# Optimization experiments

Hardware: AMD Instinct MI355X
Metric: run time of the kernel (lower is better)

The kernel has to match this reference:

```python
import jax, jax.numpy as jnp
import numpy as np

N_HEADS = 8
MAX_PARTS = 8
TOKENS_PER_PART = 64
NUM_BLOCKS = 6
D_MODEL = 256
LN_EPS = 1e-5


def layernorm(x, w, b):
    mu = jnp.mean(x, axis=-1, keepdims=True)
    var = jnp.var(x, axis=-1, keepdims=True)
    return (x - mu) * jax.lax.rsqrt(var + LN_EPS) * w + b


def mha(q, k, v, in_w, in_b, out_w, out_b):
    # torch nn.MultiheadAttention: packed in_proj [3D, D], out_proj [D, D]
    D = q.shape[-1]
    dh = D // N_HEADS
    wq, wk, wv = in_w[:D], in_w[D:2 * D], in_w[2 * D:]
    bq, bk, bv = in_b[:D], in_b[D:2 * D], in_b[2 * D:]
    qp = q @ wq.T + bq  # [B, Sq, D]
    kp = k @ wk.T + bk
    vp = v @ wv.T + bv
    B, Sq, _ = qp.shape
    Sk = kp.shape[1]
    qh = qp.reshape(B, Sq, N_HEADS, dh).transpose(0, 2, 1, 3)
    kh = kp.reshape(B, Sk, N_HEADS, dh).transpose(0, 2, 1, 3)
    vh = vp.reshape(B, Sk, N_HEADS, dh).transpose(0, 2, 1, 3)
    scores = jnp.einsum('bhqd,bhkd->bhqk', qh, kh) / jnp.sqrt(jnp.asarray(dh, qp.dtype))
    attn = jax.nn.softmax(scores, axis=-1)
    out = jnp.einsum('bhqk,bhkd->bhqd', attn, vh)
    out = out.transpose(0, 2, 1, 3).reshape(B, Sq, D)
    return out @ out_w.T + out_b


def setup_inputs() -> dict:
    key = jax.random.key(0)
    ks = jax.random.split(key, 16)
    s = 0.02
    return {
        'feat': jax.random.normal(ks[0], (64, 49, 512), jnp.float32),
        'img_proj_w': jax.random.normal(ks[1], (256, 512), jnp.float32) * s,
        'img_proj_b': jnp.zeros((256,), jnp.float32),
        'init_part_tokens': jax.random.normal(ks[2], (512, 256), jnp.float32),
        'part_id_emb': jax.random.normal(ks[3], (8, 256), jnp.float32),
        'local_in_w': jax.random.normal(ks[4], (768, 256), jnp.float32) * s,
        'local_in_b': jnp.zeros((768,), jnp.float32),
        'local_out_w': jax.random.normal(ks[5], (256, 256), jnp.float32) * s,
        'local_out_b': jnp.zeros((256,), jnp.float32),
        'cross_in_w': jax.random.normal(ks[6], (768, 256), jnp.float32) * s,
        'cross_in_b': jnp.zeros((768,), jnp.float32),
        'cross_out_w': jax.random.normal(ks[7], (256, 256), jnp.float32) * s,
        'cross_out_b': jnp.zeros((256,), jnp.float32),
        'norm1_w': jnp.ones((6, 256), jnp.float32),
        'norm1_b': jnp.zeros((6, 256), jnp.float32),
        'norm2_w': jnp.ones((6, 256), jnp.float32),
        'norm2_b': jnp.zeros((6, 256), jnp.float32),
        'coord_w': jax.random.normal(ks[8], (3, 256), jnp.float32) * s,
        'coord_b': jnp.zeros((3,), jnp.float32),
    }


def reference(feat, img_proj_w, img_proj_b, init_part_tokens, part_id_emb,
              local_in_w, local_in_b, local_out_w, local_out_b,
              cross_in_w, cross_in_b, cross_out_w, cross_out_b,
              norm1_w, norm1_b, norm2_w, norm2_b, coord_w, coord_b):
    B = feat.shape[0]
    P, T, D = MAX_PARTS, TOKENS_PER_PART, D_MODEL
    img_tokens = feat @ img_proj_w.T + img_proj_b  # [B, 49, D]
    # broadcast part-id embedding over tokens_per_part
    pid = jnp.repeat(part_id_emb, T, axis=0)  # [P*T, D]
    st = jnp.broadcast_to(init_part_tokens + pid, (B, P * T, D))
    for i in range(NUM_BLOCKS):
        # block-diagonal local attention: fold parts into batch dim
        parts = st.reshape(B * P, T, D)
        local = mha(parts, parts, parts, local_in_w, local_in_b, local_out_w, local_out_b)
        local = local.reshape(B, P * T, D)
        st = layernorm(st + local, norm1_w[i], norm1_b[i])
        cross = mha(st, img_tokens, img_tokens, cross_in_w, cross_in_b, cross_out_w, cross_out_b)
        st = layernorm(st + cross, norm2_w[i], norm2_b[i])
    coords = st @ coord_w.T + coord_b
    return coords.reshape(B, P, T, 3)
```

## Files before the change

kernel.cpp:

```cpp
#include <hip/hip_runtime.h>
#include <hip/hip_bf16.h>


#define B_     64
#define P_     8
#define T_     64
#define S_     512
#define D_     256
#define H_     8
#define DH_    32
#define NIMG_  49
#define M_ST   32768
#define M_IMG  3136
#define OSTR   264

#define AS1 __attribute__((address_space(1)))
#define AS3 __attribute__((address_space(3)))

typedef short bf16x8 __attribute__((ext_vector_type(8)));
typedef float f32x4  __attribute__((ext_vector_type(4)));

__device__ inline uint f2b_pk(float x, float y) {
    uint bx = __float_as_uint(x), by = __float_as_uint(y);
    bx = (bx + 0x7FFFu + ((bx >> 16) & 1u)) >> 16;
    by = (by + 0x7FFFu + ((by >> 16) & 1u)) >> 16;
    return bx | (by << 16);
}
__device__ inline ushort f2b(float x) {
    uint b = __float_as_uint(x);
    return (ushort)((b + 0x7FFFu + ((b >> 16) & 1u)) >> 16);
}
__device__ inline float b2f(ushort u) {
    return __uint_as_float(((uint)u) << 16);
}

__global__ __launch_bounds__(256) void cvt_bf16x4(
    const float4* __restrict__ in, uint2* __restrict__ out, int n4)
{
    int i = blockIdx.x * 256 + threadIdx.x;
    if (i < n4) {
        float4 v = in[i];
        out[i] = make_uint2(f2b_pk(v.x, v.y), f2b_pk(v.z, v.w));
    }
}

__global__ __launch_bounds__(256) void gemm_bf16(
    const ushort* __restrict__ A,
    const ushort* __restrict__ W,
    const float*  __restrict__ bias,
    ushort*       __restrict__ C,
    int M, int N, int K)
{
    __shared__ ushort smem[128 * 128];
    ushort* Asm = smem;
    ushort* Bsm = smem + 4096;

    const int tid  = threadIdx.x;
    const int lane = tid & 63;
    const int wave = tid >> 6;
    const int wr = wave >> 1, wc = wave & 1;
    const int row0 = blockIdx.x * 128, col0 = blockIdx.y * 128;

    f32x4 acc[4][4] = {};

    const int skc = (tid & 3) * 8;
    const int sr0 = tid >> 2;
    const int fr  = lane & 15;
    const int g   = lane >> 4;

    for (int k0 = 0; k0 < K; k0 += 32) {
        #pragma unroll
        for (int i = 0; i < 2; ++i) {
            const int r = sr0 + i * 64;
            const int e = (tid + i * 256) * 8;
            int ra = row0 + r; if (ra >= M) ra = M - 1;
            __builtin_amdgcn_global_load_lds(
                (const AS1 void*)(A + (size_t)ra * K + k0 + skc),
                (AS3 void*)&Asm[e], 16, 0, 0);
            __builtin_amdgcn_global_load_lds(
                (const AS1 void*)(W + (size_t)(col0 + r) * K + k0 + skc),
                (AS3 void*)&Bsm[e], 16, 0, 0);
        }
        __syncthreads();

        bf16x8 af[4], bf[4];
        #pragma unroll
        for (int i = 0; i < 4; ++i)
            af[i] = *reinterpret_cast<const bf16x8*>(&Asm[(wr * 64 + i * 16 + fr) * 32 + g * 8]);
        #pragma unroll
        for (int j = 0; j < 4; ++j)
            bf[j] = *reinterpret_cast<const bf16x8*>(&Bsm[(wc * 64 + j * 16 + fr) * 32 + g * 8]);
        #pragma unroll
        for (int i = 0; i < 4; ++i)
            #pragma unroll
            for (int j = 0; j < 4; ++j)
                acc[i][j] = __builtin_amdgcn_mfma_f32_16x16x32_bf16(
                    af[i], bf[j], acc[i][j], 0, 0, 0);
        __syncthreads();
    }

    float bn[4];
    #pragma unroll
    for (int j = 0; j < 4; ++j) bn[j] = bias[col0 + wc * 64 + j * 16 + fr];

    #pragma unroll
    for (int i = 0; i < 4; ++i)
        #pragma unroll
        for (int j = 0; j < 4; ++j)
            #pragma unroll
            for (int r = 0; r < 4; ++r)
                smem[(wr * 64 + i * 16 + g * 4 + r) * 128 + wc * 64 + j * 16 + fr] =
                    f2b(acc[i][j][r] + bn[j]);
    __syncthreads();

    #pragma unroll
    for (int it = 0; it < 8; ++it) {
        const int elem = (it * 256 + tid) * 8;
        const int lrow = elem >> 7, lcol = elem & 127;
        const int m = row0 + lrow;
        if (m < M)
            *reinterpret_cast<uint4*>(&C[(size_t)m * N + col0 + lcol]) =
                *reinterpret_cast<const uint4*>(&smem[elem]);
    }
}

__global__ __launch_bounds__(512, 4) void gemm_bf16_big(
    const ushort* __restrict__ A,
    const ushort* __restrict__ W,
    const float*  __restrict__ bias,
    ushort*       __restrict__ C,
    int N, int K)
{
    __shared__ ushort smem[16384];
    ushort* Asm = smem;
    ushort* Bsm = smem + 8192;

    const int tid  = threadIdx.x;
    const int lane = tid & 63;
    const int wave = tid >> 6;
    const int wr = wave >> 1, wc = wave & 1;
    const int row0 = blockIdx.x * 256, col0 = blockIdx.y * 128;

    f32x4 acc[4][4] = {};
    const int skc = (tid & 3) * 8;
    const int sr0 = tid >> 2;
    const int fr  = lane & 15;
    const int g   = lane >> 4;

    for (int k0 = 0; k0 < K; k0 += 32) {
        #pragma unroll
        for (int i = 0; i < 2; ++i) {
            const int r = sr0 + i * 128;
            __builtin_amdgcn_global_load_lds(
                (const AS1 void*)(A + (size_t)(row0 + r) * K + k0 + skc),
                (AS3 void*)&Asm[(tid + i * 512) * 8], 16, 0, 0);
        }
        __builtin_amdgcn_global_load_lds(
            (const AS1 void*)(W + (size_t)(col0 + sr0) * K + k0 + skc),
            (AS3 void*)&Bsm[tid * 8], 16, 0, 0);
        __syncthreads();

        bf16x8 af[4], bf[4];
        #pragma unroll
        for (int i = 0; i < 4; ++i)
            af[i] = *reinterpret_cast<const bf16x8*>(&Asm[(wr * 64 + i * 16 + fr) * 32 + g * 8]);
        #pragma unroll
        for (int j = 0; j < 4; ++j)
            bf[j] = *reinterpret_cast<const bf16x8*>(&Bsm[(wc * 64 + j * 16 + fr) * 32 + g * 8]);
        #pragma unroll
        for (int i = 0; i < 4; ++i)
            #pragma unroll
            for (int j = 0; j < 4; ++j)
                acc[i][j] = __builtin_amdgcn_mfma_f32_16x16x32_bf16(
                    af[i], bf[j], acc[i][j], 0, 0, 0);
        __syncthreads();
    }

    float bn[4];
    #pragma unroll
    for (int j = 0; j < 4; ++j) bn[j] = bias[col0 + wc * 64 + j * 16 + fr];

    #pragma unroll
    for (int h2 = 0; h2 < 2; ++h2) {
        if ((wr >> 1) == h2) {
            const int lwr = wr & 1;
            #pragma unroll
            for (int i = 0; i < 4; ++i)
                #pragma unroll
                for (int j = 0; j < 4; ++j)
                    #pragma unroll
                    for (int r = 0; r < 4; ++r)
                        smem[(lwr * 64 + i * 16 + g * 4 + r) * 128 + wc * 64 + j * 16 + fr] =
                            f2b(acc[i][j][r] + bn[j]);
        }
        __syncthreads();
        #pragma unroll
        for (int it = 0; it < 4; ++it) {
            const int elem = (it * 512 + tid) * 8;
            const int lrow = elem >> 7, lcol = elem & 127;
            *reinterpret_cast<uint4*>(
                &C[(size_t)(row0 + h2 * 128 + lrow) * N + col0 + lcol]) =
                *reinterpret_cast<const uint4*>(&smem[elem]);
        }
        __syncthreads();
    }
}

template<int CROSS>
__global__ __launch_bounds__(256) void attn_oln(
    const ushort* __restrict__ qsrc,
    const ushort* __restrict__ ksrc,
    const ushort* __restrict__ vsrc,
    const ushort* __restrict__ W,
    const float*  __restrict__ bias,
    ushort*       __restrict__ stb,
    const float*  __restrict__ lnw,
    const float*  __restrict__ lnb)
{
    constexpr int QSTR = CROSS ? 256 : 768;
    constexpr int KSTR = CROSS ? 512 : 768;

    const int bid = blockIdx.x;
    int qrow0, krow0;
    if (CROSS) { qrow0 = (bid >> 3) * 512 + (bid & 7) * 64; krow0 = (bid >> 3) * 49; }
    else       { qrow0 = bid * 64; krow0 = bid * 64; }

    __shared__ ushort P_lds[4][64][72];
    __shared__ ushort Vt_lds[4][32][72];
    __shared__ float  redS[64][4];
    __shared__ float  redS2[64][4];
    ushort* Os = &P_lds[0][0][0];
    ushort* Bs = &Vt_lds[0][0][0];

    const int tid = threadIdx.x;
    const int w = tid >> 6, l = tid & 63;
    const int fr = l & 15, g = l >> 4;
    ushort (*P)[72]  = P_lds[w];
    ushort (*Vt)[72] = Vt_lds[w];

    f32x4 o2[2][4][2] = {};

    #pragma unroll
    for (int hh = 0; hh < 2; ++hh) {
        const int h = w + hh * 4;
        const int hoff = h * 32;

        bf16x8 kf[4], qf[4];
        #pragma unroll
        for (int i = 0; i < 4; ++i) {
            int t = 16 * i + fr;
            if (CROSS && t > 48) t = 48;
            kf[i] = *reinterpret_cast<const bf16x8*>(
                ksrc + (size_t)(krow0 + t) * KSTR + hoff + g * 8);
        }
        #pragma unroll
        for (int j = 0; j < 4; ++j)
            qf[j] = *reinterpret_cast<const bf16x8*>(
                qsrc + (size_t)(qrow0 + 16 * j + fr) * QSTR + hoff + g * 8);

        #pragma unroll
        for (int t2 = 0; t2 < 2; ++t2) {
            const int task = t2 * 64 + l;
            const int rp = task >> 2, cg = task & 3;
            int r0 = 2 * rp, r1 = r0 + 1;
            if (CROSS) { if (r0 > 48) r0 = 48; if (r1 > 48) r1 = 48; }
            const uint4 a = *reinterpret_cast<const uint4*>(
                vsrc + (size_t)(krow0 + r0) * KSTR + hoff + cg * 8);
            const uint4 b = *reinterpret_cast<const uint4*>(
                vsrc + (size_t)(krow0 + r1) * KSTR + hoff + cg * 8);
            const uint ac[4] = {a.x, a.y, a.z, a.w};
            const uint bc[4] = {b.x, b.y, b.z, b.w};
            #pragma unroll
            for (int k = 0; k < 4; ++k) {
                uint lo = (ac[k] & 0xFFFFu) | (bc[k] << 16);
                uint hi = (ac[k] >> 16)     | (bc[k] & 0xFFFF0000u);
                *reinterpret_cast<uint*>(&Vt[cg * 8 + 2 * k][2 * rp])     = lo;
                *reinterpret_cast<uint*>(&Vt[cg * 8 + 2 * k + 1][2 * rp]) = hi;
            }
        }

        f32x4 st_[4][4];
        #pragma unroll
        for (int i = 0; i < 4; ++i)
            #pragma unroll
            for (int j = 0; j < 4; ++j) {
                f32x4 z = {};
                st_[i][j] = __builtin_amdgcn_mfma_f32_16x16x32_bf16(
                    kf[i], qf[j], z, 0, 0, 0);
                st_[i][j] *= 0.17677669529663689f;
            }
        if (CROSS) {
            #pragma unroll
            for (int j = 0; j < 4; ++j)
                #pragma unroll
                for (int r = 0; r < 4; ++r)
                    if (r > 0 || g > 0) st_[3][j][r] = -1e30f;
        }

        #pragma unroll
        for (int j = 0; j < 4; ++j) {
            float mx = -1e30f;
            #pragma unroll
            for (int i = 0; i < 4; ++i)
                #pragma unroll
                for (int r = 0; r < 4; ++r) mx = fmaxf(mx, st_[i][j][r]);
            mx = fmaxf(mx, __shfl_xor(mx, 16));
            mx = fmaxf(mx, __shfl_xor(mx, 32));
            float sm = 0.f;
            #pragma unroll
            for (int i = 0; i < 4; ++i)
                #pragma unroll
                for (int r = 0; r < 4; ++r) {
                    float p = __expf(st_[i][j][r] - mx);
                    st_[i][j][r] = p;
                    sm += p;
                }
            sm += __shfl_xor(sm, 16);
            sm += __shfl_xor(sm, 32);
            const float inv = 1.f / sm;
            const int q = 16 * j + fr;
            #pragma unroll
            for (int i = 0; i < 4; ++i) {
                uint lo = f2b_pk(st_[i][j][0] * inv, st_[i][j][1] * inv);
                uint hi = f2b_pk(st_[i][j][2] * inv, st_[i][j][3] * inv);
                *reinterpret_cast<uint2*>(&P[q][16 * i + 4 * g]) = make_uint2(lo, hi);
            }
        }

        __syncthreads();

        #pragma unroll
        for (int s = 0; s < 2; ++s) {
            bf16x8 pa[4], vb[2];
            #pragma unroll
            for (int i = 0; i < 4; ++i)
                pa[i] = *reinterpret_cast<const bf16x8*>(&P[16 * i + fr][32 * s + 8 * g]);
            #pragma unroll
            for (int j2 = 0; j2 < 2; ++j2)
                vb[j2] = *reinterpret_cast<const bf16x8*>(&Vt[16 * j2 + fr][32 * s + 8 * g]);
            #pragma unroll
            for (int i = 0; i < 4; ++i)
                #pragma unroll
                for (int j2 = 0; j2 < 2; ++j2)
                    o2[hh][i][j2] = __builtin_amdgcn_mfma_f32_16x16x32_bf16(
                        pa[i], vb[j2], o2[hh][i][j2], 0, 0, 0);
        }
    }

    __syncthreads();

    #pragma unroll
    for (int hh = 0; hh < 2; ++hh)
        #pragma unroll
        for (int i = 0; i < 4; ++i)
            #pragma unroll
            for (int j2 = 0; j2 < 2; ++j2)
                #pragma unroll
                for (int r = 0; r < 4; ++r)
                    Os[(16 * i + 4 * g + r) * OSTR + hh * 128 + w * 32 + 16 * j2 + fr] =
                        f2b(o2[hh][i][j2][r]);

    const int skc = (tid & 3) * 8;
    const int srB = tid >> 2;

    f32x4 acc[4][4] = {};
    for (int k0 = 0; k0 < 256; k0 += 32) {
        #pragma unroll
        for (int q = 0; q < 4; ++q)
            __builtin_amdgcn_global_load_lds(
                (const AS1 void*)(W + (size_t)(srB + q * 64) * 256 + k0 + skc),
                (AS3 void*)&Bs[(tid + q * 256) * 8], 16, 0, 0);
        __syncthreads();

        bf16x8 af[4], bf[4];
        #pragma unroll
        for (int i = 0; i < 4; ++i)
            af[i] = *reinterpret_cast<const bf16x8*>(&Os[(i * 16 + fr) * OSTR + k0 + g * 8]);
        #pragma unroll
        for (int j = 0; j < 4; ++j)
            bf[j] = *reinterpret_cast<const bf16x8*>(&Bs[(w * 64 + j * 16 + fr) * 32 + g * 8]);
        #pragma unroll
        for (int i = 0; i < 4; ++i)
            #pragma unroll
            for (int j = 0; j < 4; ++j)
                acc[i][j] = __builtin_amdgcn_mfma_f32_16x16x32_bf16(
                    af[i], bf[j], acc[i][j], 0, 0, 0);
        __syncthreads();
    }

    int   col[4]; float bv[4], wv[4], lb[4];
    #pragma unroll
    for (int j = 0; j < 4; ++j) {
        col[j] = w * 64 + j * 16 + fr;
        bv[j]  = bias[col[j]];
        wv[j]  = lnw[col[j]];
        lb[j]  = lnb[col[j]];
    }

    const int row0 = qrow0;

    #pragma unroll
    for (int i = 0; i < 4; ++i)
        #pragma unroll
        for (int r = 0; r < 4; ++r) {
            const int rl = i * 16 + g * 4 + r;
            const size_t rb = (size_t)(row0 + rl) * 256;
            float s = 0.f, s2 = 0.f;
            #pragma unroll
            for (int j = 0; j < 4; ++j) {
                float x = acc[i][j][r] + bv[j] + b2f(stb[rb + col[j]]);
                acc[i][j][r] = x;
                s += x; s2 += x * x;
            }
            #pragma unroll
            for (int o = 1; o < 16; o <<= 1) {
                s  += __shfl_xor(s, o);
                s2 += __shfl_xor(s2, o);
            }
            if (fr == 0) { redS[rl][w] = s; redS2[rl][w] = s2; }
        }
    __syncthreads();

    #pragma unroll
    for (int i = 0; i < 4; ++i)
        #pragma unroll
        for (int r = 0; r < 4; ++r) {
            const int rl = i * 16 + g * 4 + r;
            const float ts  = redS[rl][0] + redS[rl][1] + redS[rl][2] + redS[rl][3];
            const float ts2 = redS2[rl][0] + redS2[rl][1] + redS2[rl][2] + redS2[rl][3];
            const float mean = ts * (1.f / 256.f);
            const float var  = ts2 * (1.f / 256.f) - mean * mean;
            const float rs   = rsqrtf(var + 1e-5f);
            #pragma unroll
            for (int j = 0; j < 4; ++j) {
                const float y = (acc[i][j][r] - mean) * rs * wv[j] + lb[j];
                Os[rl * OSTR + col[j]] = f2b(y);
            }
        }
    __syncthreads();

    #pragma unroll
    for (int it = 0; it < 8; ++it) {
        const int e = it * 256 + tid;
        const int lrow = e >> 5, lcol = (e & 31) * 8;
        *reinterpret_cast<uint4*>(&stb[(size_t)(row0 + lrow) * 256 + lcol]) =
            *reinterpret_cast<const uint4*>(&Os[lrow * OSTR + lcol]);
    }
}

__global__ __launch_bounds__(256) void init_st(
    ushort* __restrict__ stb,
    const float* __restrict__ init_tokens, const float* __restrict__ pid_emb)
{
    int i = blockIdx.x * 256 + threadIdx.x;
    int c = i & 63;
    int s = (i >> 6) & 511;
    int p = s >> 6;
    float4 v = *reinterpret_cast<const float4*>(&init_tokens[s * 256 + c * 4]);
    float4 e = *reinterpret_cast<const float4*>(&pid_emb[p * 256 + c * 4]);
    v.x += e.x; v.y += e.y; v.z += e.z; v.w += e.w;
    *reinterpret_cast<uint2*>(&stb[(size_t)i * 4]) =
        make_uint2(f2b_pk(v.x, v.y), f2b_pk(v.z, v.w));
}

__global__ __launch_bounds__(256) void coord_head(
    const ushort* __restrict__ stb, const float* __restrict__ w,
    const float* __restrict__ b, float* __restrict__ out)
{
    const int row = blockIdx.x * 8 + (threadIdx.x >> 5);
    const int l   = threadIdx.x & 31;
    const ushort* x = stb + (size_t)row * 256 + l * 8;
    uint4 xv = *reinterpret_cast<const uint4*>(x);
    float xf[8];
    const uint xc[4] = {xv.x, xv.y, xv.z, xv.w};
    #pragma unroll
    for (int k = 0; k < 4; ++k) {
        xf[2*k]   = __uint_as_float(xc[k] << 16);
        xf[2*k+1] = __uint_as_float(xc[k] & 0xFFFF0000u);
    }
    float acc[3];
    #pragma unroll
    for (int n = 0; n < 3; ++n) {
        const float* wn = w + n * 256 + l * 8;
        float4 w0 = *reinterpret_cast<const float4*>(wn);
        float4 w1 = *reinterpret_cast<const float4*>(wn + 4);
        acc[n] = xf[0]*w0.x + xf[1]*w0.y + xf[2]*w0.z + xf[3]*w0.w
               + xf[4]*w1.x + xf[5]*w1.y + xf[6]*w1.z + xf[7]*w1.w;
    }
    #pragma unroll
    for (int o = 16; o; o >>= 1)
        #pragma unroll
        for (int n = 0; n < 3; ++n) acc[n] += __shfl_xor(acc[n], o);
    if (l == 0) {
        #pragma unroll
        for (int n = 0; n < 3; ++n) out[(size_t)row * 3 + n] = acc[n] + b[n];
    }
}

extern "C" void kernel_launch(void* const* d_in, const int* in_sizes, int n_in,
                              void* d_out, int out_size, void* d_ws, size_t ws_size,
                              hipStream_t stream)
{
    const float* feat             = (const float*)d_in[0];
    const float* img_proj_w      = (const float*)d_in[1];
    const float* img_proj_b      = (const float*)d_in[2];
    const float* init_part_tokens = (const float*)d_in[3];
    const float* part_id_emb     = (const float*)d_in[4];
    const float* local_in_w      = (const float*)d_in[5];
    const float* local_in_b      = (const float*)d_in[6];
    const float* local_out_w     = (const float*)d_in[7];
    const float* local_out_b     = (const float*)d_in[8];
    const float* cross_in_w      = (const float*)d_in[9];
    const float* cross_in_b      = (const float*)d_in[10];
    const float* cross_out_w     = (const float*)d_in[11];
    const float* cross_out_b     = (const float*)d_in[12];
    const float* norm1_w         = (const float*)d_in[13];
    const float* norm1_b         = (const float*)d_in[14];
    const float* norm2_w         = (const float*)d_in[15];
    const float* norm2_b         = (const float*)d_in[16];
    const float* coord_w         = (const float*)d_in[17];
    const float* coord_b         = (const float*)d_in[18];
    float* out = (float*)d_out;

    ushort* stb  = (ushort*)d_ws;
    ushort* big  = stb  + (size_t)M_ST * D_;
    ushort* kv   = big  + (size_t)M_ST * 3 * D_;
    ushort* fbf  = kv   + (size_t)M_IMG * 512;
    ushort* img  = fbf  + (size_t)M_IMG * 512;
    ushort* lw_in  = img   + (size_t)M_IMG * D_;
    ushort* lw_out = lw_in  + 768 * 256;
    ushort* cw_in  = lw_out + 256 * 256;
    ushort* cw_out = cw_in  + 768 * 256;
    ushort* iw     = cw_out + 256 * 256;

    cvt_bf16x4<<<768*256/4/256, 256, 0, stream>>>((const float4*)local_in_w,  (uint2*)lw_in,  768*256/4);
    cvt_bf16x4<<<256*256/4/256, 256, 0, stream>>>((const float4*)local_out_w, (uint2*)lw_out, 256*256/4);
    cvt_bf16x4<<<768*256/4/256, 256, 0, stream>>>((const float4*)cross_in_w,  (uint2*)cw_in,  768*256/4);
    cvt_bf16x4<<<256*256/4/256, 256, 0, stream>>>((const float4*)cross_out_w, (uint2*)cw_out, 256*256/4);
    cvt_bf16x4<<<256*512/4/256, 256, 0, stream>>>((const float4*)img_proj_w,  (uint2*)iw,     256*512/4);
    cvt_bf16x4<<<(M_IMG*512/4 + 255)/256, 256, 0, stream>>>((const float4*)feat, (uint2*)fbf, M_IMG*512/4);

    gemm_bf16<<<dim3((M_IMG+127)/128, 2), 256, 0, stream>>>(fbf, iw, img_proj_b, img, M_IMG, 256, 512);
    gemm_bf16<<<dim3((M_IMG+127)/128, 4), 256, 0, stream>>>(
        img, cw_in + 256*256, cross_in_b + 256, kv, M_IMG, 512, 256);
    init_st<<<M_ST * D_ / 4 / 256, 256, 0, stream>>>(stb, init_part_tokens, part_id_emb);

    for (int i = 0; i < 6; ++i) {
        gemm_bf16_big<<<dim3(M_ST/256, 6), 512, 0, stream>>>(stb, lw_in, local_in_b, big, 768, 256);
        attn_oln<0><<<512, 256, 0, stream>>>(big, big + 256, big + 512,
                                             lw_out, local_out_b, stb,
                                             norm1_w + i*256, norm1_b + i*256);
        gemm_bf16_big<<<dim3(M_ST/256, 2), 512, 0, stream>>>(stb, cw_in, cross_in_b, big, 256, 256);
        attn_oln<1><<<512, 256, 0, stream>>>(big, kv, kv + 256,
                                             cw_out, cross_out_b, stb,
                                             norm2_w + i*256, norm2_b + i*256);
    }

    coord_head<<<M_ST / 8, 256, 0, stream>>>(stb, coord_w, coord_b, out);
}
```

Baseline: 659.8 us.

## Fuse feat fp32-to-bf16 conversion into image projection GEMM and prefetch out-proj weights

```diff
diff --git a/kernel.cpp b/kernel.cpp
--- a/kernel.cpp
+++ b/kernel.cpp
@@ -124,6 +124,92 @@
     }
 }
 
+__global__ __launch_bounds__(256) void gemm_bf16_a32(
+    const float*  __restrict__ A,
+    const ushort* __restrict__ W,
+    const float*  __restrict__ bias,
+    ushort*       __restrict__ C,
+    int M, int N, int K)
+{
+    __shared__ ushort smem[128 * 128];
+    ushort* Asm = smem;
+    ushort* Bsm = smem + 4096;
+
+    const int tid  = threadIdx.x;
+    const int lane = tid & 63;
+    const int wave = tid >> 6;
+    const int wr = wave >> 1, wc = wave & 1;
+    const int row0 = blockIdx.x * 128, col0 = blockIdx.y * 128;
+
+    f32x4 acc[4][4] = {};
+
+    const int skc = (tid & 3) * 8;
+    const int sr0 = tid >> 2;
+    const int fr  = lane & 15;
+    const int g   = lane >> 4;
+
+    for (int k0 = 0; k0 < K; k0 += 32) {
+        #pragma unroll
+        for (int i = 0; i < 2; ++i) {
+            const int r = sr0 + i * 64;
+            const int e = (tid + i * 256) * 8;
+            int ra = row0 + r; if (ra >= M) ra = M - 1;
+            const float* ga = A + (size_t)ra * K + k0 + skc;
+            float4 v0 = *reinterpret_cast<const float4*>(ga);
+            float4 v1 = *reinterpret_cast<const float4*>(ga + 4);
+            uint4 pk;
+            pk.x = f2b_pk(v0.x, v0.y);
+            pk.y = f2b_pk(v0.z, v0.w);
+            pk.z = f2b_pk(v1.x, v1.y);
+            pk.w = f2b_pk(v1.z, v1.w);
+            *reinterpret_cast<uint4*>(&Asm[e]) = pk;
+            __builtin_amdgcn_global_load_lds(
+                (const AS1 void*)(W + (size_t)(col0 + r) * K + k0 + skc),
+                (AS3 void*)&Bsm[e], 16, 0, 0);
+        }
+        __syncthreads();
+
+        bf16x8 af[4], bf[4];
+        #pragma unroll
+        for (int i = 0; i < 4; ++i)
+            af[i] = *reinterpret_cast<const bf16x8*>(&Asm[(wr * 64 + i * 16 + fr) * 32 + g * 8]);
+        #pragma unroll
+        for (int j = 0; j < 4; ++j)
+            bf[j] = *reinterpret_cast<const bf16x8*>(&Bsm[(wc * 64 + j * 16 + fr) * 32 + g * 8]);
+        #pragma unroll
+        for (int i = 0; i < 4; ++i)
+            #pragma unroll
+            for (int j = 0; j < 4; ++j)
+                acc[i][j] = __builtin_amdgcn_mfma_f32_16x16x32_bf16(
+                    af[i], bf[j], acc[i][j], 0, 0, 0);
+        __syncthreads();
+    }
+
+    float bn[4];
+    #pragma unroll
+    for (int j = 0; j < 4; ++j) bn[j] = bias[col0 + wc * 64 + j * 16 + fr];
+
+    #pragma unroll
+    for (int i = 0; i < 4; ++i)
+        #pragma unroll
+        for (int j = 0; j < 4; ++j)
+            #pragma unroll
+            for (int r = 0; r < 4; ++r)
+                smem[(wr * 64 + i * 16 + g * 4 + r) * 128 + wc * 64 + j * 16 + fr] =
+                    f2b(acc[i][j][r] + bn[j]);
+    __syncthreads();
+
+    #pragma unroll
+    for (int it = 0; it < 8; ++it) {
+        const int elem = (it * 256 + tid) * 8;
+        const int lrow = elem >> 7, lcol = elem & 127;
+        const int m = row0 + lrow;
+        if (m < M)
+            *reinterpret_cast<uint4*>(&C[(size_t)m * N + col0 + lcol]) =
+                *reinterpret_cast<const uint4*>(&smem[elem]);
+    }
+}
+
 __global__ __launch_bounds__(512, 4) void gemm_bf16_big(
     const ushort* __restrict__ A,
     const ushort* __restrict__ W,
@@ -347,6 +433,14 @@
         }
     }
 
+    const int skc = (tid & 3) * 8;
+    const int srB = tid >> 2;
+    uint4 wreg[4];
+    #pragma unroll
+    for (int q = 0; q < 4; ++q)
+        wreg[q] = *reinterpret_cast<const uint4*>(
+            W + (size_t)(srB + q * 64) * 256 + skc);
+
     __syncthreads();
 
     #pragma unroll
@@ -360,16 +454,19 @@
                     Os[(16 * i + 4 * g + r) * OSTR + hh * 128 + w * 32 + 16 * j2 + fr] =
                         f2b(o2[hh][i][j2][r]);
 
-    const int skc = (tid & 3) * 8;
-    const int srB = tid >> 2;
-
     f32x4 acc[4][4] = {};
-    for (int k0 = 0; k0 < 256; k0 += 32) {
+    #pragma unroll
+    for (int k0i = 0; k0i < 8; ++k0i) {
+        const int k0 = k0i * 32;
         #pragma unroll
         for (int q = 0; q < 4; ++q)
-            __builtin_amdgcn_global_load_lds(
-                (const AS1 void*)(W + (size_t)(srB + q * 64) * 256 + k0 + skc),
-                (AS3 void*)&Bs[(tid + q * 256) * 8], 16, 0, 0);
+            *reinterpret_cast<uint4*>(&Bs[(tid + q * 256) * 8]) = wreg[q];
+        if (k0i < 7) {
+            #pragma unroll
+            for (int q = 0; q < 4; ++q)
+                wreg[q] = *reinterpret_cast<const uint4*>(
+                    W + (size_t)(srB + q * 64) * 256 + (k0 + 32) + skc);
+        }
         __syncthreads();
 
         bf16x8 af[4], bf[4];
@@ -525,8 +622,7 @@
     ushort* stb  = (ushort*)d_ws;
     ushort* big  = stb  + (size_t)M_ST * D_;
     ushort* kv   = big  + (size_t)M_ST * 3 * D_;
-    ushort* fbf  = kv   + (size_t)M_IMG * 512;
-    ushort* img  = fbf  + (size_t)M_IMG * 512;
+    ushort* img  = kv   + (size_t)M_IMG * 512;
     ushort* lw_in  = img   + (size_t)M_IMG * D_;
     ushort* lw_out = lw_in  + 768 * 256;
     ushort* cw_in  = lw_out + 256 * 256;
@@ -538,9 +634,9 @@
     cvt_bf16x4<<<768*256/4/256, 256, 0, stream>>>((const float4*)cross_in_w,  (uint2*)cw_in,  768*256/4);
     cvt_bf16x4<<<256*256/4/256, 256, 0, stream>>>((const float4*)cross_out_w, (uint2*)cw_out, 256*256/4);
     cvt_bf16x4<<<256*512/4/256, 256, 0, stream>>>((const float4*)img_proj_w,  (uint2*)iw,     256*512/4);
-    cvt_bf16x4<<<(M_IMG*512/4 + 255)/256, 256, 0, stream>>>((const float4*)feat, (uint2*)fbf, M_IMG*512/4);
-
-    gemm_bf16<<<dim3((M_IMG+127)/128, 2), 256, 0, stream>>>(fbf, iw, img_proj_b, img, M_IMG, 256, 512);
+
+    gemm_bf16_a32<<<dim3((M_IMG+127)/128, 2), 256, 0, stream>>>(
+        feat, iw, img_proj_b, img, M_IMG, 256, 512);
     gemm_bf16<<<dim3((M_IMG+127)/128, 4), 256, 0, stream>>>(
         img, cw_in + 256*256, cross_in_b + 256, kv, M_IMG, 512, 256);
     init_st<<<M_ST * D_ / 4 / 256, 256, 0, stream>>>(stb, init_part_tokens, part_id_emb);
```

Measured after the change: 837.8 us. 1.27x slower.
